# Kernel tuning notes

Hardware: AMD Instinct MI355X
Metric: run time of the kernel (lower is better)

## Reference

```python
import jax, jax.numpy as jnp
import numpy as np

T, B, C, HS, RD = 32, 32, 128, 512, 3  # timesteps, batch, state_channels, hidden_size, recurse_depth
HW = 7


def setup_inputs() -> dict:
    key = jax.random.key(0)
    ks = jax.random.split(key, 6)
    x = jax.random.normal(ks[0], (T * B, C, HW, HW), jnp.float32)
    hxs = jax.random.normal(ks[1], (B, 2 * C, HW, HW), jnp.float32)
    masks = jax.random.uniform(ks[2], (T * B,), jnp.float32)
    # ConvLSTMCell: conv over concat(x, h) [2C in] -> 4C gate channels, 3x3, bias
    Wconv = jax.random.normal(ks[3], (4 * C, 2 * C, 3, 3), jnp.float32) * 0.02
    bconv = jnp.zeros((4 * C,), jnp.float32)
    # flat_lin: Linear(C*7*7 -> hidden_size), torch layout [out, in]
    Wlin = jax.random.normal(ks[4], (HS, C * HW * HW), jnp.float32) * 0.02
    blin = jnp.zeros((HS,), jnp.float32)
    return {"x": x, "hxs": hxs, "masks": masks, "Wconv": Wconv, "bconv": bconv, "Wlin": Wlin, "blin": blin}


def reference(x, hxs, masks, Wconv, bconv, Wlin, blin):
    xs = x.reshape(T, B, C, HW, HW)
    ms = masks.reshape(T, B)
    h0, c0 = hxs[:, :C], hxs[:, C:]

    def conv_gates(inp):  # [B, 2C, 7, 7] -> [B, 4C, 7, 7]
        y = jax.lax.conv_general_dilated(
            inp, Wconv, window_strides=(1, 1), padding="SAME",
            dimension_numbers=("NCHW", "OIHW", "NCHW"))
        return y + bconv[None, :, None, None]

    def step(carry, inp):
        h, c = carry
        x_t, m_t = inp
        m = m_t[:, None, None, None]
        h = h * m
        c = c * m
        for _ in range(RD):  # recurse_depth inner unroll (sequential dependency)
            g = conv_gates(jnp.concatenate([x_t, h], axis=1))
            cc_i, cc_f, cc_o, cc_g = jnp.split(g, 4, axis=1)
            i = jax.nn.sigmoid(cc_i)
            f = jax.nn.sigmoid(cc_f)
            o = jax.nn.sigmoid(cc_o)
            gg = jnp.tanh(cc_g)
            c = f * c + i * gg
            h = o * jnp.tanh(c)
        out = jax.nn.relu(c.reshape(B, -1) @ Wlin.T + blin)  # flat_lin applied to c
        return (h, c), out

    (hT, cT), outs = jax.lax.scan(step, (h0, c0), (xs, ms))
    return outs.reshape(T * B, HS), jnp.concatenate([hT, cT], axis=1)
```

## Files before the change

### kernel.cpp

```cpp
#include <hip/hip_runtime.h>
#include <hip/hip_bf16.h>
#include <stdint.h>

#define T_  32
#define B_  32
#define C_  128
#define HS_ 512
#define HW_ 7
#define S_  49
#define CS_  (C_*S_)
#define ICS_ (2*C_*S_)
#define KH_  1152
#define KL_  6272
#define M_   1568
#define MR_  1600
#define N_   512

typedef __attribute__((ext_vector_type(8))) short short8;
typedef __attribute__((ext_vector_type(4))) float f32x4;
typedef __hip_bfloat16 bf16;

union bfbits { bf16 b; short s; };

__device__ __forceinline__ void gl16(const void* g, void* l) {
    __builtin_amdgcn_global_load_lds((const __attribute__((address_space(1))) void*)g,
                                     (__attribute__((address_space(3))) void*)l, 16, 0, 0);
}

__device__ __forceinline__ float sigm_f(float v) { return 1.0f / (1.0f + __expf(-v)); }
__device__ __forceinline__ float tanh_f(float v) { return 1.0f - 2.0f / (__expf(2.0f * v) + 1.0f); }

#define PIPE_BARRIER_COUNTED()  do {                                   \
    asm volatile("s_waitcnt vmcnt(8)" ::: "memory");                   \
    __builtin_amdgcn_sched_barrier(0);                                 \
    __builtin_amdgcn_s_barrier();                                      \
    __builtin_amdgcn_sched_barrier(0);                                 \
} while (0)
#define PIPE_BARRIER_DRAIN()  do {                                     \
    asm volatile("s_waitcnt vmcnt(0)" ::: "memory");                   \
    __builtin_amdgcn_sched_barrier(0);                                 \
    __builtin_amdgcn_s_barrier();                                      \
    __builtin_amdgcn_sched_barrier(0);                                 \
} while (0)

__global__ __launch_bounds__(256, 1) void k_fgemm(
    const bf16* __restrict__ xTt, const bf16* __restrict__ hT,
    bf16* __restrict__ hTN,
    const bf16* __restrict__ WxP, const bf16* __restrict__ WhP,
    const float* __restrict__ bconv,
    float* __restrict__ Gx, float* __restrict__ cbuf,
    const float* __restrict__ mask_c, const float* __restrict__ mask_a,
    bf16* __restrict__ chist_t, const bf16* __restrict__ zb, int mode0)
{
    __shared__ __align__(16) uint8_t smem[98304];
    bf16* sA = (bf16*)smem;
    bf16* sB = (bf16*)(smem + 49152);
    float (*gld)[68] = (float(*)[68])smem;

    const int tid = threadIdx.x, lane = tid & 63, w = tid >> 6;
    const int wr = w >> 1, wc = w & 1;
    const int m0 = blockIdx.x * 64, n0 = blockIdx.y * 64;

    const int kq = tid & 15, rr = tid >> 4;
    const int swz = ((kq ^ rr) << 3);
    int abS[4], ay[4], ax[4]; bool rok[4];
#pragma unroll
    for (int q = 0; q < 4; ++q) {
        int ra = m0 + q * 16 + rr;
        rok[q] = ra < M_;
        int b = ra / S_, s = ra - b * S_;
        abS[q] = b * S_;
        ay[q] = s / HW_; ax[q] = s - ay[q] * HW_;
    }

    const int NS = mode0 ? 18 : 9;

    f32x4 accX[2][2], accH[2][2];
    if (mode0) {
#pragma unroll
        for (int fn = 0; fn < 2; ++fn) {
            int np = n0 + wc * 32 + fn * 16 + (lane & 15);
            float bv = bconv[((np & 3) << 7) + (np >> 2)];
            f32x4 b4 = {bv, bv, bv, bv};
            accX[0][fn] = b4; accX[1][fn] = b4;
            f32x4 z4 = {0.f, 0.f, 0.f, 0.f};
            accH[0][fn] = z4; accH[1][fn] = z4;
        }
    } else {
#pragma unroll
        for (int fm = 0; fm < 2; ++fm) {
            int row = m0 + wr * 32 + fm * 16 + ((lane >> 4) << 2);
#pragma unroll
            for (int fn = 0; fn < 2; ++fn) {
                int col = n0 + wc * 32 + fn * 16 + (lane & 15);
#pragma unroll
                for (int j = 0; j < 4; ++j)
                    accH[fm][fn][j] = Gx[(size_t)(row + j) * N_ + col];
            }
        }
    }

    auto stage = [&](int st, int dbuf) {
        int xph = (mode0 && st < 9);
        int kid = xph ? st : (mode0 ? st - 9 : st);
        int ky = kid / 3, kx = kid - ky * 3;
        const bf16* Asrc = xph ? xTt : hT;
        const bf16* Wsrc = xph ? WxP : WhP;
        bf16* lA = sA + dbuf * 8192;
        bf16* lB = sB + dbuf * 8192;
#pragma unroll
        for (int q = 0; q < 4; ++q) {
            int y2 = ay[q] + ky - 1, x2 = ax[q] + kx - 1;
            const bf16* rb = (rok[q] && (unsigned)y2 < (unsigned)HW_ && (unsigned)x2 < (unsigned)HW_)
                ? Asrc + (((size_t)(abS[q] + y2 * HW_ + x2)) << 7) : zb;
            gl16(rb + swz, lA + q * 2048 + w * 512);
            gl16(Wsrc + (size_t)(n0 + q * 16 + rr) * KH_ + kid * 128 + swz, lB + q * 2048 + w * 512);
        }
    };

    auto compute = [&](int dbuf, f32x4 (&acc)[2][2]) {
        const bf16* lA = sA + dbuf * 8192;
        const bf16* lB = sB + dbuf * 8192;
        short8 af[2][4], bq[2][4];
#pragma unroll
        for (int kh = 0; kh < 4; ++kh) {
            int c = kh * 4 + (lane >> 4);
            int xr = (c ^ (lane & 15)) << 3;
#pragma unroll
            for (int fm = 0; fm < 2; ++fm) {
                int r = wr * 32 + fm * 16 + (lane & 15);
                af[fm][kh] = *(const short8*)(lA + r * 128 + xr);
            }
#pragma unroll
            for (int fn = 0; fn < 2; ++fn) {
                int r = wc * 32 + fn * 16 + (lane & 15);
                bq[fn][kh] = *(const short8*)(lB + r * 128 + xr);
            }
        }
#pragma unroll
        for (int kh = 0; kh < 4; ++kh)
#pragma unroll
            for (int fm = 0; fm < 2; ++fm)
#pragma unroll
                for (int fn = 0; fn < 2; ++fn)
                    acc[fm][fn] = __builtin_amdgcn_mfma_f32_16x16x32_bf16(
                        af[fm][kh], bq[fn][kh], acc[fm][fn], 0, 0, 0);
    };

    stage(0, 0);
    stage(1, 1);
    PIPE_BARRIER_COUNTED();

    int cur = 0;
#pragma unroll 1
    for (int st = 0; st < NS; ++st) {
        int pre = cur + 2; if (pre >= 3) pre -= 3;
        if (st + 2 < NS) stage(st + 2, pre);
        if (mode0 && st < 9) compute(cur, accX);
        else                 compute(cur, accH);
        if (st + 2 < NS) { PIPE_BARRIER_COUNTED(); }
        else             { PIPE_BARRIER_DRAIN(); }
        ++cur; if (cur == 3) cur = 0;
    }
    __syncthreads();

    if (mode0) {
#pragma unroll
        for (int fm = 0; fm < 2; ++fm) {
            int row = m0 + wr * 32 + fm * 16 + ((lane >> 4) << 2);
#pragma unroll
            for (int fn = 0; fn < 2; ++fn) {
                int col = n0 + wc * 32 + fn * 16 + (lane & 15);
#pragma unroll
                for (int j = 0; j < 4; ++j) {
                    Gx[(size_t)(row + j) * N_ + col] = accX[fm][fn][j];
                    accH[fm][fn][j] += accX[fm][fn][j];
                }
            }
        }
    }

#pragma unroll
    for (int fm = 0; fm < 2; ++fm)
#pragma unroll
        for (int fn = 0; fn < 2; ++fn) {
            int row = wr * 32 + fm * 16 + ((lane >> 4) << 2);
            int col = wc * 32 + fn * 16 + (lane & 15);
#pragma unroll
            for (int j = 0; j < 4; ++j) gld[row + j][col] = accH[fm][fn][j];
        }
    __syncthreads();

#pragma unroll
    for (int q2 = 0; q2 < 4; ++q2) {
        int e = tid + q2 * 256;
        int row = e >> 4, cc = e & 15;
        int m = m0 + row;
        if (m >= M_) continue;
        int b = m / S_, s = m - b * S_;
        int cg = (n0 >> 2) + cc;
        float g0 = gld[row][cc * 4 + 0], g1 = gld[row][cc * 4 + 1];
        float g2 = gld[row][cc * 4 + 2], g3 = gld[row][cc * 4 + 3];
        float ig = sigm_f(g0);
        float fg = sigm_f(g1);
        float og = sigm_f(g2);
        float gg = tanh_f(g3);
        size_t ci = (((size_t)b * S_ + s) << 7) + cg;
        float co = cbuf[ci];
        if (mask_c) co *= mask_c[b];
        float cn = fg * co + ig * gg;
        cbuf[ci] = cn;
        float hn = og * tanh_f(cn);
        float am = mask_a ? mask_a[b] : 1.f;
        hTN[ci] = __float2bfloat16(hn * am);
        if (chist_t) chist_t[(size_t)b * KL_ + s * C_ + cg] = __float2bfloat16(cn);
    }
}

__global__ __launch_bounds__(256, 1) void k_lingemm(
    const bf16* __restrict__ Ac, const bf16* __restrict__ Wl,
    const float* __restrict__ blin, float* __restrict__ out)
{
    __shared__ __align__(16) uint8_t smem[98304];
    bf16* sA = (bf16*)smem;
    bf16* sB = (bf16*)(smem + 49152);

    const int tid = threadIdx.x, lane = tid & 63, w = tid >> 6;
    const int wr = w >> 1, wc = w & 1;
    const int m0 = blockIdx.x * 64, n0 = blockIdx.y * 64;
    const int kq = tid & 15, rr = tid >> 4;
    const int swz = ((kq ^ rr) << 3);

    f32x4 acc[2][2];
#pragma unroll
    for (int fn = 0; fn < 2; ++fn) {
        int np = n0 + wc * 32 + fn * 16 + (lane & 15);
        float bv = blin[np];
        f32x4 b4 = {bv, bv, bv, bv};
        acc[0][fn] = b4; acc[1][fn] = b4;
    }

    auto stage = [&](int st, int dbuf) {
        bf16* lA = sA + dbuf * 8192;
        bf16* lB = sB + dbuf * 8192;
#pragma unroll
        for (int q = 0; q < 4; ++q) {
            gl16(Ac + (size_t)(m0 + q * 16 + rr) * KL_ + st * 128 + swz, lA + q * 2048 + w * 512);
            gl16(Wl + (size_t)(n0 + q * 16 + rr) * KL_ + st * 128 + swz, lB + q * 2048 + w * 512);
        }
    };
    auto compute = [&](int dbuf) {
        const bf16* lA = sA + dbuf * 8192;
        const bf16* lB = sB + dbuf * 8192;
        short8 af[2][4], bq[2][4];
#pragma unroll
        for (int kh = 0; kh < 4; ++kh) {
            int c = kh * 4 + (lane >> 4);
            int xr = (c ^ (lane & 15)) << 3;
#pragma unroll
            for (int fm = 0; fm < 2; ++fm) {
                int r = wr * 32 + fm * 16 + (lane & 15);
                af[fm][kh] = *(const short8*)(lA + r * 128 + xr);
            }
#pragma unroll
            for (int fn = 0; fn < 2; ++fn) {
                int r = wc * 32 + fn * 16 + (lane & 15);
                bq[fn][kh] = *(const short8*)(lB + r * 128 + xr);
            }
        }
#pragma unroll
        for (int kh = 0; kh < 4; ++kh)
#pragma unroll
            for (int fm = 0; fm < 2; ++fm)
#pragma unroll
                for (int fn = 0; fn < 2; ++fn)
                    acc[fm][fn] = __builtin_amdgcn_mfma_f32_16x16x32_bf16(
                        af[fm][kh], bq[fn][kh], acc[fm][fn], 0, 0, 0);
    };

    stage(0, 0);
    stage(1, 1);
    PIPE_BARRIER_COUNTED();

    int cur = 0;
#pragma unroll 1
    for (int st = 0; st < 49; ++st) {
        int pre = cur + 2; if (pre >= 3) pre -= 3;
        if (st + 2 < 49) stage(st + 2, pre);
        compute(cur);
        if (st + 2 < 49) { PIPE_BARRIER_COUNTED(); }
        else             { PIPE_BARRIER_DRAIN(); }
        ++cur; if (cur == 3) cur = 0;
    }

#pragma unroll
    for (int fm = 0; fm < 2; ++fm)
#pragma unroll
        for (int fn = 0; fn < 2; ++fn) {
            int col = n0 + wc * 32 + fn * 16 + (lane & 15);
            int rb  = m0 + wr * 32 + fm * 16 + ((lane >> 4) << 2);
#pragma unroll
            for (int j = 0; j < 4; ++j)
                out[(size_t)(rb + j) * N_ + col] = fmaxf(acc[fm][fn][j], 0.f);
        }
}

__global__ __launch_bounds__(256) void k_wsplit(const float* __restrict__ Wc,
                                               bf16* __restrict__ WxP, bf16* __restrict__ WhP) {
    int idx = blockIdx.x * 256 + threadIdx.x;
    if (idx >= 512 * 288) return;
    int np = idx / 288, kq = idx % 288;
    int oc = ((np & 3) << 7) + (np >> 2);
    int kk = kq * 8;
    int half = kk >= KH_;
    int krel = kk - half * KH_;
    short8 v;
#pragma unroll
    for (int j = 0; j < 8; ++j) {
        int kr = krel + j;
        int kid = kr >> 7, ic = (kr & 127) + half * 128;
        bfbits bb; bb.b = __float2bfloat16(Wc[((size_t)oc * 256 + ic) * 9 + kid]);
        v[j] = bb.s;
    }
    bf16* dst = half ? WhP : WxP;
    *reinterpret_cast<short8*>(dst + (size_t)np * KH_ + krel) = v;
}

__global__ __launch_bounds__(256) void k_wlin2(const float* __restrict__ Wl, bf16* __restrict__ Wp) {
    int idx = blockIdx.x * 256 + threadIdx.x;
    if (idx >= 512 * 784) return;
    int np = idx / 784, kq = idx % 784;
    short8 v;
#pragma unroll
    for (int j = 0; j < 8; ++j) {
        int kp = kq * 8 + j;
        int s = kp >> 7, c = kp & 127;
        bfbits bb; bb.b = __float2bfloat16(Wl[(size_t)np * KL_ + c * S_ + s]);
        v[j] = bb.s;
    }
    *reinterpret_cast<short8*>(Wp + (size_t)np * KL_ + kq * 8) = v;
}

__global__ __launch_bounds__(256) void k_xpose(const float* __restrict__ x, bf16* __restrict__ xT) {
    int idx = blockIdx.x * 256 + threadIdx.x;
    if (idx >= 1024 * 784) return;
    int r = idx / 784;
    int rem = idx % 784;
    int s = rem / 16, c8 = (rem & 15) * 8;
    const float* sp = x + (size_t)r * CS_ + c8 * S_ + s;
    short8 v;
#pragma unroll
    for (int j = 0; j < 8; ++j) { bfbits bb; bb.b = __float2bfloat16(sp[j * S_]); v[j] = bb.s; }
    *reinterpret_cast<short8*>(xT + (((size_t)r * S_ + s) << 7) + c8) = v;
}

__global__ __launch_bounds__(256) void k_hcprep(const float* __restrict__ hxs,
                                                const float* __restrict__ mask0,
                                                bf16* __restrict__ hT, float* __restrict__ cbuf) {
    int idx = blockIdx.x * 256 + threadIdx.x;
    if (idx >= 32 * 784) return;
    int b = idx / 784;
    int rem = idx % 784;
    int s = rem / 16, c8 = (rem & 15) * 8;
    float m = mask0[b];
    const float* hp = hxs + (size_t)b * ICS_ + c8 * S_ + s;
    const float* cp = hp + CS_;
    size_t o = (((size_t)b * S_ + s) << 7) + c8;
    short8 v;
#pragma unroll
    for (int j = 0; j < 8; ++j) {
        bfbits bb; bb.b = __float2bfloat16(hp[j * S_] * m); v[j] = bb.s;
        cbuf[o + j] = cp[j * S_];
    }
    *reinterpret_cast<short8*>(hT + o) = v;
}

__global__ __launch_bounds__(256) void k_zero16(uint4* __restrict__ p, int n) {
    int i = blockIdx.x * 256 + threadIdx.x;
    if (i < n) p[i] = make_uint4(0, 0, 0, 0);
}

__global__ __launch_bounds__(256) void k_final(const bf16* __restrict__ hT, const float* __restrict__ cbuf,
                                               float* __restrict__ out) {
    int i = blockIdx.x * 256 + threadIdx.x;
    if (i >= B_ * ICS_) return;
    int b = i / ICS_, r = i % ICS_;
    int ch = r / S_, s = r % S_;
    size_t o = (((size_t)b * S_ + s) << 7);
    out[i] = (ch < C_) ? __bfloat162float(hT[o + ch]) : cbuf[o + (ch - C_)];
}

extern "C" void kernel_launch(void* const* d_in, const int* in_sizes, int n_in,
                              void* d_out, int out_size, void* d_ws, size_t ws_size,
                              hipStream_t stream) {
    (void)in_sizes; (void)n_in; (void)out_size; (void)ws_size;
    const float* x     = (const float*)d_in[0];
    const float* hxs   = (const float*)d_in[1];
    const float* masks = (const float*)d_in[2];
    const float* Wconv = (const float*)d_in[3];
    const float* bconv = (const float*)d_in[4];
    const float* Wlin  = (const float*)d_in[5];
    const float* blin  = (const float*)d_in[6];
    float* out = (float*)d_out;

    uint8_t* p = (uint8_t*)d_ws;
    bf16* WxP   = (bf16*)p;   p += (size_t)512 * KH_ * 2;
    bf16* WhP   = (bf16*)p;   p += (size_t)512 * KH_ * 2;
    bf16* Wlp   = (bf16*)p;   p += (size_t)512 * KL_ * 2;
    bf16* xT    = (bf16*)p;   p += (size_t)1024 * S_ * C_ * 2;
    bf16* hA    = (bf16*)p;   p += (size_t)B_ * S_ * C_ * 2;
    bf16* hB    = (bf16*)p;   p += (size_t)B_ * S_ * C_ * 2;
    float* cbuf = (float*)p;  p += (size_t)B_ * S_ * C_ * 4;
    float* Gx   = (float*)p;  p += (size_t)MR_ * N_ * 4;
    bf16* chist = (bf16*)p;   p += (size_t)1024 * KL_ * 2;
    bf16* zb    = (bf16*)p;   p += 1024;
    bf16* hbufs[2] = {hA, hB};

    k_wsplit<<<576, 256, 0, stream>>>(Wconv, WxP, WhP);
    k_wlin2<<<1568, 256, 0, stream>>>(Wlin, Wlp);
    k_xpose<<<3136, 256, 0, stream>>>(x, xT);
    k_hcprep<<<98, 256, 0, stream>>>(hxs, masks, hA, cbuf);
    k_zero16<<<1, 256, 0, stream>>>((uint4*)zb, 64);

    int g = 0;
    for (int t = 0; t < T_; ++t) {
        const bf16* xTt = xT + (size_t)t * B_ * S_ * C_;
        for (int rd = 0; rd < 3; ++rd) {
            const float* mc = (rd == 0) ? masks + (size_t)t * B_ : nullptr;
            const float* ma = (rd == 2 && t < T_ - 1) ? masks + (size_t)(t + 1) * B_ : nullptr;
            bf16* ct = (rd == 2) ? chist + (size_t)t * B_ * KL_ : nullptr;
            k_fgemm<<<dim3(25, 8), 256, 0, stream>>>(
                (rd == 0) ? xTt : nullptr, hbufs[g & 1], hbufs[(g + 1) & 1],
                WxP, WhP, bconv, Gx, cbuf, mc, ma, ct, zb, (rd == 0) ? 1 : 0);
            ++g;
        }
    }

    k_lingemm<<<dim3(16, 8), 256, 0, stream>>>(chist, Wlp, blin, out);
    k_final<<<1568, 256, 0, stream>>>(hbufs[0], cbuf, out + (size_t)T_ * B_ * HS_);
}
```

Before: 1.464 ms.

## Replace per-step conv-LSTM launches with persistent kernel using grid barrier

Replaces the 96 separate fused conv-gate GEMM launches with one persistent kernel of 200 blocks. Each block keeps its slice of the recurrent weights resident in shared memory, holds its cell state and x-gate partial sums in registers, and synchronises with the other blocks through an atomic sense-reversing grid barrier. This removes per-launch overhead, the Gx round trips to global memory and re-staging of the weights on every step. In exchange the A operands now load directly from global memory without an LDS pipeline, and correctness relies on all 200 blocks being co-resident, since otherwise the spin barrier deadlocks.

```diff
diff --git a/kernel.cpp b/kernel.cpp
--- a/kernel.cpp
+++ b/kernel.cpp
@@ -13,8 +13,8 @@
 #define KH_  1152
 #define KL_  6272
 #define M_   1568
-#define MR_  1600
 #define N_   512
+#define NBLK_ 200
 
 typedef __attribute__((ext_vector_type(8))) short short8;
 typedef __attribute__((ext_vector_type(4))) float f32x4;
@@ -29,6 +29,231 @@
 
 __device__ __forceinline__ float sigm_f(float v) { return 1.0f / (1.0f + __expf(-v)); }
 __device__ __forceinline__ float tanh_f(float v) { return 1.0f - 2.0f / (__expf(2.0f * v) + 1.0f); }
+__device__ __forceinline__ float sel4(float r0, float r1, float r2, float r3, int idx) {
+    float a = (idx & 1) ? r1 : r0;
+    float b = (idx & 1) ? r3 : r2;
+    return (idx & 2) ? b : a;
+}
+
+__device__ __forceinline__ void grid_barrier(int* cnt, int* sense, int want) {
+    __threadfence();
+    __syncthreads();
+    if (threadIdx.x == 0) {
+        int v = __hip_atomic_fetch_add(cnt, 1, __ATOMIC_ACQ_REL, __HIP_MEMORY_SCOPE_AGENT);
+        if (v == NBLK_ - 1) {
+            __hip_atomic_store(cnt, 0, __ATOMIC_RELAXED, __HIP_MEMORY_SCOPE_AGENT);
+            __hip_atomic_store(sense, want, __ATOMIC_RELEASE, __HIP_MEMORY_SCOPE_AGENT);
+        } else {
+            while (__hip_atomic_load(sense, __ATOMIC_ACQUIRE, __HIP_MEMORY_SCOPE_AGENT) != want)
+                __builtin_amdgcn_s_sleep(16);
+        }
+    }
+    __syncthreads();
+}
+
+__global__ __launch_bounds__(256, 1) void k_persist(
+    const bf16* __restrict__ xT, bf16* __restrict__ h0, bf16* __restrict__ h1,
+    const bf16* __restrict__ WxP, const bf16* __restrict__ WhP,
+    const float* __restrict__ bconv, const float* __restrict__ cbuf,
+    const float* __restrict__ masks, bf16* __restrict__ chist,
+    float* __restrict__ outS, const bf16* __restrict__ zb, int* __restrict__ bar)
+{
+    __shared__ __align__(16) bf16 sWh[64 * KH_];
+
+    const int tid = threadIdx.x, lane = tid & 63, w = tid >> 6;
+    const int wr = w >> 1, wc = w & 1;
+    const int bid = blockIdx.x;
+    const int m0 = (bid >> 3) * 64, n0 = (bid & 7) * 64;
+
+#pragma unroll
+    for (int i = 0; i < 36; ++i) {
+        int ci = i * 256 + tid;
+        int col = ci / 144, s = ci - col * 144;
+        int sc = s ^ (col & 7);
+        gl16(WhP + (size_t)(n0 + col) * KH_ + sc * 8, sWh + (size_t)ci * 8);
+    }
+
+    int abase[2], ayy[2], axx[2]; bool aok[2];
+#pragma unroll
+    for (int fm = 0; fm < 2; ++fm) {
+        int ra = m0 + wr * 32 + fm * 16 + (lane & 15);
+        aok[fm] = ra < M_;
+        int b = ra / S_, s = ra - b * S_;
+        abase[fm] = b * S_;
+        ayy[fm] = s / HW_; axx[fm] = s - ayy[fm] * HW_;
+    }
+    const int aco = ((lane >> 4) << 3);
+
+    int ebc[2], esc[2], ebase[2]; bool eok[2];
+#pragma unroll
+    for (int fm = 0; fm < 2; ++fm) {
+        int er = m0 + wr * 32 + fm * 16 + ((lane >> 4) << 2) + (lane & 3);
+        eok[fm] = er < M_;
+        int b = er / S_, s = er - b * S_;
+        if (b > B_ - 1) b = B_ - 1;
+        ebc[fm] = b; esc[fm] = s; ebase[fm] = b * S_ + s;
+    }
+    int chn[2];
+#pragma unroll
+    for (int fn = 0; fn < 2; ++fn)
+        chn[fn] = (n0 >> 2) + wc * 8 + fn * 4 + ((lane & 15) >> 2);
+
+    float cst[2][2];
+#pragma unroll
+    for (int fm = 0; fm < 2; ++fm)
+#pragma unroll
+        for (int fn = 0; fn < 2; ++fn)
+            cst[fm][fn] = cbuf[((size_t)ebase[fm] << 7) + chn[fn]];
+
+    float bias[2];
+#pragma unroll
+    for (int fn = 0; fn < 2; ++fn) {
+        int np = n0 + wc * 32 + fn * 16 + (lane & 15);
+        bias[fn] = bconv[((np & 3) << 7) + (np >> 2)];
+    }
+
+    asm volatile("s_waitcnt vmcnt(0)" ::: "memory");
+    __syncthreads();
+
+    auto ldA = [&](const bf16* src, int kid, int fm, int kh) -> short8 {
+        int ky = kid / 3, kx = kid - 3 * (kid / 3);
+        int y2 = ayy[fm] + ky - 1, x2 = axx[fm] + kx - 1;
+        bool ok = aok[fm] && (unsigned)y2 < (unsigned)HW_ && (unsigned)x2 < (unsigned)HW_;
+        const bf16* p = ok ? src + (((size_t)(abase[fm] + y2 * HW_ + x2)) << 7) + kh * 32 + aco
+                           : zb;
+        return *(const short8*)p;
+    };
+    auto ldB = [&](int kid, int fn, int kh) -> short8 {
+        int col = wc * 32 + fn * 16 + (lane & 15);
+        int chunk = kid * 16 + kh * 4 + (lane >> 4);
+        int phys = chunk ^ (col & 7);
+        return *(const short8*)(sWh + col * KH_ + phys * 8);
+    };
+    auto ldBx = [&](int kid, int fn, int kh) -> short8 {
+        int col = n0 + wc * 32 + fn * 16 + (lane & 15);
+        return *(const short8*)(WxP + (size_t)col * KH_ + kid * 128 + kh * 32 + aco);
+    };
+
+    auto gemmH = [&](const bf16* hsrc, f32x4 (&acc)[2][2]) {
+#pragma unroll
+        for (int kid = 0; kid < 9; ++kid) {
+            short8 af[2][4], bq[2][4];
+#pragma unroll
+            for (int kh = 0; kh < 4; ++kh) {
+#pragma unroll
+                for (int fm = 0; fm < 2; ++fm) af[fm][kh] = ldA(hsrc, kid, fm, kh);
+#pragma unroll
+                for (int fn = 0; fn < 2; ++fn) bq[fn][kh] = ldB(kid, fn, kh);
+            }
+#pragma unroll
+            for (int kh = 0; kh < 4; ++kh)
+#pragma unroll
+                for (int fm = 0; fm < 2; ++fm)
+#pragma unroll
+                    for (int fn = 0; fn < 2; ++fn)
+                        acc[fm][fn] = __builtin_amdgcn_mfma_f32_16x16x32_bf16(
+                            af[fm][kh], bq[fn][kh], acc[fm][fn], 0, 0, 0);
+        }
+    };
+    auto gemmX = [&](const bf16* xsrc, f32x4 (&acc)[2][2]) {
+#pragma unroll
+        for (int kid = 0; kid < 9; ++kid) {
+            short8 af[2][4], bq[2][4];
+#pragma unroll
+            for (int kh = 0; kh < 4; ++kh) {
+#pragma unroll
+                for (int fm = 0; fm < 2; ++fm) af[fm][kh] = ldA(xsrc, kid, fm, kh);
+#pragma unroll
+                for (int fn = 0; fn < 2; ++fn) bq[fn][kh] = ldBx(kid, fn, kh);
+            }
+#pragma unroll
+            for (int kh = 0; kh < 4; ++kh)
+#pragma unroll
+                for (int fm = 0; fm < 2; ++fm)
+#pragma unroll
+                    for (int fn = 0; fn < 2; ++fn)
+                        acc[fm][fn] = __builtin_amdgcn_mfma_f32_16x16x32_bf16(
+                            af[fm][kh], bq[fn][kh], acc[fm][fn], 0, 0, 0);
+        }
+    };
+
+    const bf16* hcur = h0;
+    bf16* hnxt = h1;
+    f32x4 gx[2][2];
+    const int j = lane & 3;
+    int want = 1;
+
+#pragma unroll 1
+    for (int t = 0; t < T_; ++t) {
+        const bf16* xTt = xT + (size_t)t * (B_ * S_ * C_);
+#pragma unroll 1
+        for (int rd = 0; rd < 3; ++rd) {
+            f32x4 acc[2][2];
+            if (rd == 0) {
+#pragma unroll
+                for (int fm = 0; fm < 2; ++fm)
+#pragma unroll
+                    for (int fn = 0; fn < 2; ++fn) {
+                        f32x4 b4 = {bias[fn], bias[fn], bias[fn], bias[fn]};
+                        acc[fm][fn] = b4;
+                    }
+                gemmX(xTt, acc);
+#pragma unroll
+                for (int fm = 0; fm < 2; ++fm)
+#pragma unroll
+                    for (int fn = 0; fn < 2; ++fn) gx[fm][fn] = acc[fm][fn];
+                gemmH(hcur, acc);
+            } else {
+#pragma unroll
+                for (int fm = 0; fm < 2; ++fm)
+#pragma unroll
+                    for (int fn = 0; fn < 2; ++fn) acc[fm][fn] = gx[fm][fn];
+                gemmH(hcur, acc);
+            }
+
+            const bool last = (t == T_ - 1) && (rd == 2);
+#pragma unroll
+            for (int fm = 0; fm < 2; ++fm) {
+                float mc = 1.f, ma = 1.f;
+                if (rd == 0) mc = masks[t * B_ + ebc[fm]];
+                if (rd == 2 && t < T_ - 1) ma = masks[(t + 1) * B_ + ebc[fm]];
+#pragma unroll
+                for (int fn = 0; fn < 2; ++fn) {
+                    f32x4 a = acc[fm][fn];
+                    float s0 = sel4(a[0], a[1], a[2], a[3], j);
+                    float s1 = __shfl_xor(sel4(a[0], a[1], a[2], a[3], j ^ 1), 1);
+                    float s2 = __shfl_xor(sel4(a[0], a[1], a[2], a[3], j ^ 2), 2);
+                    float s3 = __shfl_xor(sel4(a[0], a[1], a[2], a[3], j ^ 3), 3);
+                    float gi = sel4(s0, s1, s2, s3, j);
+                    float gf = sel4(s0, s1, s2, s3, j ^ 1);
+                    float go = sel4(s0, s1, s2, s3, j ^ 2);
+                    float gg = sel4(s0, s1, s2, s3, j ^ 3);
+                    float ig = sigm_f(gi), fg = sigm_f(gf), og = sigm_f(go), gv = tanh_f(gg);
+                    float c = cst[fm][fn];
+                    if (rd == 0) c *= mc;
+                    float cn = fg * c + ig * gv;
+                    cst[fm][fn] = cn;
+                    float hn = og * tanh_f(cn);
+                    if (eok[fm]) {
+                        int ch = chn[fn];
+                        if (!last)
+                            hnxt[((size_t)ebase[fm] << 7) + ch] = __float2bfloat16(hn * ma);
+                        if (rd == 2)
+                            chist[((size_t)t * B_ + ebc[fm]) * KL_ + esc[fm] * C_ + ch] =
+                                __float2bfloat16(cn);
+                        if (last) {
+                            outS[(size_t)ebc[fm] * ICS_ + ch * S_ + esc[fm]] = hn;
+                            outS[(size_t)ebc[fm] * ICS_ + (C_ + ch) * S_ + esc[fm]] = cn;
+                        }
+                    }
+                }
+            }
+
+            if (!last) { grid_barrier(bar, bar + 1, want); want ^= 1; }
+            const bf16* tmp = hcur; hcur = hnxt; hnxt = (bf16*)tmp;
+        }
+    }
+}
 
 #define PIPE_BARRIER_COUNTED()  do {                                   \
     asm volatile("s_waitcnt vmcnt(8)" ::: "memory");                   \
@@ -43,180 +268,6 @@
     __builtin_amdgcn_sched_barrier(0);                                 \
 } while (0)
 
-__global__ __launch_bounds__(256, 1) void k_fgemm(
-    const bf16* __restrict__ xTt, const bf16* __restrict__ hT,
-    bf16* __restrict__ hTN,
-    const bf16* __restrict__ WxP, const bf16* __restrict__ WhP,
-    const float* __restrict__ bconv,
-    float* __restrict__ Gx, float* __restrict__ cbuf,
-    const float* __restrict__ mask_c, const float* __restrict__ mask_a,
-    bf16* __restrict__ chist_t, const bf16* __restrict__ zb, int mode0)
-{
-    __shared__ __align__(16) uint8_t smem[98304];
-    bf16* sA = (bf16*)smem;
-    bf16* sB = (bf16*)(smem + 49152);
-    float (*gld)[68] = (float(*)[68])smem;
-
-    const int tid = threadIdx.x, lane = tid & 63, w = tid >> 6;
-    const int wr = w >> 1, wc = w & 1;
-    const int m0 = blockIdx.x * 64, n0 = blockIdx.y * 64;
-
-    const int kq = tid & 15, rr = tid >> 4;
-    const int swz = ((kq ^ rr) << 3);
-    int abS[4], ay[4], ax[4]; bool rok[4];
-#pragma unroll
-    for (int q = 0; q < 4; ++q) {
-        int ra = m0 + q * 16 + rr;
-        rok[q] = ra < M_;
-        int b = ra / S_, s = ra - b * S_;
-        abS[q] = b * S_;
-        ay[q] = s / HW_; ax[q] = s - ay[q] * HW_;
-    }
-
-    const int NS = mode0 ? 18 : 9;
-
-    f32x4 accX[2][2], accH[2][2];
-    if (mode0) {
-#pragma unroll
-        for (int fn = 0; fn < 2; ++fn) {
-            int np = n0 + wc * 32 + fn * 16 + (lane & 15);
-            float bv = bconv[((np & 3) << 7) + (np >> 2)];
-            f32x4 b4 = {bv, bv, bv, bv};
-            accX[0][fn] = b4; accX[1][fn] = b4;
-            f32x4 z4 = {0.f, 0.f, 0.f, 0.f};
-            accH[0][fn] = z4; accH[1][fn] = z4;
-        }
-    } else {
-#pragma unroll
-        for (int fm = 0; fm < 2; ++fm) {
-            int row = m0 + wr * 32 + fm * 16 + ((lane >> 4) << 2);
-#pragma unroll
-            for (int fn = 0; fn < 2; ++fn) {
-                int col = n0 + wc * 32 + fn * 16 + (lane & 15);
-#pragma unroll
-                for (int j = 0; j < 4; ++j)
-                    accH[fm][fn][j] = Gx[(size_t)(row + j) * N_ + col];
-            }
-        }
-    }
-
-    auto stage = [&](int st, int dbuf) {
-        int xph = (mode0 && st < 9);
-        int kid = xph ? st : (mode0 ? st - 9 : st);
-        int ky = kid / 3, kx = kid - ky * 3;
-        const bf16* Asrc = xph ? xTt : hT;
-        const bf16* Wsrc = xph ? WxP : WhP;
-        bf16* lA = sA + dbuf * 8192;
-        bf16* lB = sB + dbuf * 8192;
-#pragma unroll
-        for (int q = 0; q < 4; ++q) {
-            int y2 = ay[q] + ky - 1, x2 = ax[q] + kx - 1;
-            const bf16* rb = (rok[q] && (unsigned)y2 < (unsigned)HW_ && (unsigned)x2 < (unsigned)HW_)
-                ? Asrc + (((size_t)(abS[q] + y2 * HW_ + x2)) << 7) : zb;
-            gl16(rb + swz, lA + q * 2048 + w * 512);
-            gl16(Wsrc + (size_t)(n0 + q * 16 + rr) * KH_ + kid * 128 + swz, lB + q * 2048 + w * 512);
-        }
-    };
-
-    auto compute = [&](int dbuf, f32x4 (&acc)[2][2]) {
-        const bf16* lA = sA + dbuf * 8192;
-        const bf16* lB = sB + dbuf * 8192;
-        short8 af[2][4], bq[2][4];
-#pragma unroll
-        for (int kh = 0; kh < 4; ++kh) {
-            int c = kh * 4 + (lane >> 4);
-            int xr = (c ^ (lane & 15)) << 3;
-#pragma unroll
-            for (int fm = 0; fm < 2; ++fm) {
-                int r = wr * 32 + fm * 16 + (lane & 15);
-                af[fm][kh] = *(const short8*)(lA + r * 128 + xr);
-            }
-#pragma unroll
-            for (int fn = 0; fn < 2; ++fn) {
-                int r = wc * 32 + fn * 16 + (lane & 15);
-                bq[fn][kh] = *(const short8*)(lB + r * 128 + xr);
-            }
-        }
-#pragma unroll
-        for (int kh = 0; kh < 4; ++kh)
-#pragma unroll
-            for (int fm = 0; fm < 2; ++fm)
-#pragma unroll
-                for (int fn = 0; fn < 2; ++fn)
-                    acc[fm][fn] = __builtin_amdgcn_mfma_f32_16x16x32_bf16(
-                        af[fm][kh], bq[fn][kh], acc[fm][fn], 0, 0, 0);
-    };
-
-    stage(0, 0);
-    stage(1, 1);
-    PIPE_BARRIER_COUNTED();
-
-    int cur = 0;
-#pragma unroll 1
-    for (int st = 0; st < NS; ++st) {
-        int pre = cur + 2; if (pre >= 3) pre -= 3;
-        if (st + 2 < NS) stage(st + 2, pre);
-        if (mode0 && st < 9) compute(cur, accX);
-        else                 compute(cur, accH);
-        if (st + 2 < NS) { PIPE_BARRIER_COUNTED(); }
-        else             { PIPE_BARRIER_DRAIN(); }
-        ++cur; if (cur == 3) cur = 0;
-    }
-    __syncthreads();
-
-    if (mode0) {
-#pragma unroll
-        for (int fm = 0; fm < 2; ++fm) {
-            int row = m0 + wr * 32 + fm * 16 + ((lane >> 4) << 2);
-#pragma unroll
-            for (int fn = 0; fn < 2; ++fn) {
-                int col = n0 + wc * 32 + fn * 16 + (lane & 15);
-#pragma unroll
-                for (int j = 0; j < 4; ++j) {
-                    Gx[(size_t)(row + j) * N_ + col] = accX[fm][fn][j];
-                    accH[fm][fn][j] += accX[fm][fn][j];
-                }
-            }
-        }
-    }
-
-#pragma unroll
-    for (int fm = 0; fm < 2; ++fm)
-#pragma unroll
-        for (int fn = 0; fn < 2; ++fn) {
-            int row = wr * 32 + fm * 16 + ((lane >> 4) << 2);
-            int col = wc * 32 + fn * 16 + (lane & 15);
-#pragma unroll
-            for (int j = 0; j < 4; ++j) gld[row + j][col] = accH[fm][fn][j];
-        }
-    __syncthreads();
-
-#pragma unroll
-    for (int q2 = 0; q2 < 4; ++q2) {
-        int e = tid + q2 * 256;
-        int row = e >> 4, cc = e & 15;
-        int m = m0 + row;
-        if (m >= M_) continue;
-        int b = m / S_, s = m - b * S_;
-        int cg = (n0 >> 2) + cc;
-        float g0 = gld[row][cc * 4 + 0], g1 = gld[row][cc * 4 + 1];
-        float g2 = gld[row][cc * 4 + 2], g3 = gld[row][cc * 4 + 3];
-        float ig = sigm_f(g0);
-        float fg = sigm_f(g1);
-        float og = sigm_f(g2);
-        float gg = tanh_f(g3);
-        size_t ci = (((size_t)b * S_ + s) << 7) + cg;
-        float co = cbuf[ci];
-        if (mask_c) co *= mask_c[b];
-        float cn = fg * co + ig * gg;
-        cbuf[ci] = cn;
-        float hn = og * tanh_f(cn);
-        float am = mask_a ? mask_a[b] : 1.f;
-        hTN[ci] = __float2bfloat16(hn * am);
-        if (chist_t) chist_t[(size_t)b * KL_ + s * C_ + cg] = __float2bfloat16(cn);
-    }
-}
-
 __global__ __launch_bounds__(256, 1) void k_lingemm(
     const bf16* __restrict__ Ac, const bf16* __restrict__ Wl,
     const float* __restrict__ blin, float* __restrict__ out)
@@ -300,8 +351,8 @@
             int col = n0 + wc * 32 + fn * 16 + (lane & 15);
             int rb  = m0 + wr * 32 + fm * 16 + ((lane >> 4) << 2);
 #pragma unroll
-            for (int j = 0; j < 4; ++j)
-                out[(size_t)(rb + j) * N_ + col] = fmaxf(acc[fm][fn][j], 0.f);
+            for (int jj = 0; jj < 4; ++jj)
+                out[(size_t)(rb + jj) * N_ + col] = fmaxf(acc[fm][fn][jj], 0.f);
         }
 }
 
@@ -316,11 +367,11 @@
     int krel = kk - half * KH_;
     short8 v;
 #pragma unroll
-    for (int j = 0; j < 8; ++j) {
-        int kr = krel + j;
+    for (int jj = 0; jj < 8; ++jj) {
+        int kr = krel + jj;
         int kid = kr >> 7, ic = (kr & 127) + half * 128;
         bfbits bb; bb.b = __float2bfloat16(Wc[((size_t)oc * 256 + ic) * 9 + kid]);
-        v[j] = bb.s;
+        v[jj] = bb.s;
     }
     bf16* dst = half ? WhP : WxP;
     *reinterpret_cast<short8*>(dst + (size_t)np * KH_ + krel) = v;
@@ -332,11 +383,11 @@
     int np = idx / 784, kq = idx % 784;
     short8 v;
 #pragma unroll
-    for (int j = 0; j < 8; ++j) {
-        int kp = kq * 8 + j;
+    for (int jj = 0; jj < 8; ++jj) {
+        int kp = kq * 8 + jj;
         int s = kp >> 7, c = kp & 127;
         bfbits bb; bb.b = __float2bfloat16(Wl[(size_t)np * KL_ + c * S_ + s]);
-        v[j] = bb.s;
+        v[jj] = bb.s;
     }
     *reinterpret_cast<short8*>(Wp + (size_t)np * KL_ + kq * 8) = v;
 }
@@ -350,7 +401,7 @@
     const float* sp = x + (size_t)r * CS_ + c8 * S_ + s;
     short8 v;
 #pragma unroll
-    for (int j = 0; j < 8; ++j) { bfbits bb; bb.b = __float2bfloat16(sp[j * S_]); v[j] = bb.s; }
+    for (int jj = 0; jj < 8; ++jj) { bfbits bb; bb.b = __float2bfloat16(sp[jj * S_]); v[jj] = bb.s; }
     *reinterpret_cast<short8*>(xT + (((size_t)r * S_ + s) << 7) + c8) = v;
 }
 
@@ -368,9 +419,9 @@
     size_t o = (((size_t)b * S_ + s) << 7) + c8;
     short8 v;
 #pragma unroll
-    for (int j = 0; j < 8; ++j) {
-        bfbits bb; bb.b = __float2bfloat16(hp[j * S_] * m); v[j] = bb.s;
-        cbuf[o + j] = cp[j * S_];
+    for (int jj = 0; jj < 8; ++jj) {
+        bfbits bb; bb.b = __float2bfloat16(hp[jj * S_] * m); v[jj] = bb.s;
+        cbuf[o + jj] = cp[jj * S_];
     }
     *reinterpret_cast<short8*>(hT + o) = v;
 }
@@ -378,16 +429,6 @@
 __global__ __launch_bounds__(256) void k_zero16(uint4* __restrict__ p, int n) {
     int i = blockIdx.x * 256 + threadIdx.x;
     if (i < n) p[i] = make_uint4(0, 0, 0, 0);
-}
-
-__global__ __launch_bounds__(256) void k_final(const bf16* __restrict__ hT, const float* __restrict__ cbuf,
-                                               float* __restrict__ out) {
-    int i = blockIdx.x * 256 + threadIdx.x;
-    if (i >= B_ * ICS_) return;
-    int b = i / ICS_, r = i % ICS_;
-    int ch = r / S_, s = r % S_;
-    size_t o = (((size_t)b * S_ + s) << 7);
-    out[i] = (ch < C_) ? __bfloat162float(hT[o + ch]) : cbuf[o + (ch - C_)];
 }
 
 extern "C" void kernel_launch(void* const* d_in, const int* in_sizes, int n_in,
@@ -411,31 +452,19 @@
     bf16* hA    = (bf16*)p;   p += (size_t)B_ * S_ * C_ * 2;
     bf16* hB    = (bf16*)p;   p += (size_t)B_ * S_ * C_ * 2;
     float* cbuf = (float*)p;  p += (size_t)B_ * S_ * C_ * 4;
-    float* Gx   = (float*)p;  p += (size_t)MR_ * N_ * 4;
     bf16* chist = (bf16*)p;   p += (size_t)1024 * KL_ * 2;
     bf16* zb    = (bf16*)p;   p += 1024;
-    bf16* hbufs[2] = {hA, hB};
+    int*  bar   = (int*)p;    p += 1024;
 
     k_wsplit<<<576, 256, 0, stream>>>(Wconv, WxP, WhP);
     k_wlin2<<<1568, 256, 0, stream>>>(Wlin, Wlp);
     k_xpose<<<3136, 256, 0, stream>>>(x, xT);
     k_hcprep<<<98, 256, 0, stream>>>(hxs, masks, hA, cbuf);
-    k_zero16<<<1, 256, 0, stream>>>((uint4*)zb, 64);
-
-    int g = 0;
-    for (int t = 0; t < T_; ++t) {
-        const bf16* xTt = xT + (size_t)t * B_ * S_ * C_;
-        for (int rd = 0; rd < 3; ++rd) {
-            const float* mc = (rd == 0) ? masks + (size_t)t * B_ : nullptr;
-            const float* ma = (rd == 2 && t < T_ - 1) ? masks + (size_t)(t + 1) * B_ : nullptr;
-            bf16* ct = (rd == 2) ? chist + (size_t)t * B_ * KL_ : nullptr;
-            k_fgemm<<<dim3(25, 8), 256, 0, stream>>>(
-                (rd == 0) ? xTt : nullptr, hbufs[g & 1], hbufs[(g + 1) & 1],
-                WxP, WhP, bconv, Gx, cbuf, mc, ma, ct, zb, (rd == 0) ? 1 : 0);
-            ++g;
-        }
-    }
+    k_zero16<<<1, 256, 0, stream>>>((uint4*)zb, 128);
+
+    k_persist<<<dim3(NBLK_), dim3(256), 0, stream>>>(
+        xT, hA, hB, WxP, WhP, bconv, cbuf, masks, chist,
+        out + (size_t)T_ * B_ * HS_, zb, bar);
 
     k_lingemm<<<dim3(16, 8), 256, 0, stream>>>(chist, Wlp, blin, out);
-    k_final<<<1568, 256, 0, stream>>>(hbufs[0], cbuf, out + (size_t)T_ * B_ * HS_);
-}
+}
```

Result: slower. 4.905 ms (+235.1%).

## Stage whole batch-row halo in LDS and read weights directly from global

Applied to the files above, without the earlier changes.

Each block now loads all input rows for its batches (up to 147 spatial rows plus a zero row) into LDS once, instead of doing a per-tap im2col gather through a triple-buffered pipeline. The 3x3 taps then index LDS directly. Weights are read straight from global/L2 into registers rather than staged through LDS. The gate epilogue uses lane shuffles in place of an LDS round trip, and the separate zero-buffer kernel is removed. The risks are exposed global weight-load latency with no software pipelining, and a larger LDS footprint that may change occupancy.

```diff
diff --git a/kernel.cpp b/kernel.cpp
--- a/kernel.cpp
+++ b/kernel.cpp
@@ -15,6 +15,7 @@
 #define M_   1568
 #define MR_  1600
 #define N_   512
+#define ZROW_ 147
 
 typedef __attribute__((ext_vector_type(8))) short short8;
 typedef __attribute__((ext_vector_type(4))) float f32x4;
@@ -29,6 +30,178 @@
 
 __device__ __forceinline__ float sigm_f(float v) { return 1.0f / (1.0f + __expf(-v)); }
 __device__ __forceinline__ float tanh_f(float v) { return 1.0f - 2.0f / (__expf(2.0f * v) + 1.0f); }
+__device__ __forceinline__ float sel4(float r0, float r1, float r2, float r3, int idx) {
+    float a = (idx & 1) ? r1 : r0;
+    float b = (idx & 1) ? r3 : r2;
+    return (idx & 2) ? b : a;
+}
+
+__global__ __launch_bounds__(256) void k_fgemm(
+    const bf16* __restrict__ xTt, const bf16* __restrict__ hT,
+    bf16* __restrict__ hTN,
+    const bf16* __restrict__ WxP, const bf16* __restrict__ WhP,
+    const float* __restrict__ bconv,
+    float* __restrict__ Gx, float* __restrict__ cbuf,
+    const float* __restrict__ mask_c, const float* __restrict__ mask_a,
+    bf16* __restrict__ chist_t, int mode0)
+{
+    __shared__ __align__(16) bf16 sH[148 * 128];
+    __shared__ __align__(16) bf16 sX[148 * 128];
+
+    const int tid = threadIdx.x, lane = tid & 63, w = tid >> 6;
+    const int wr = w >> 1, wc = w & 1;
+    const int m0 = blockIdx.x * 64, n0 = blockIdx.y * 64;
+    const int bA = m0 / S_;
+
+#pragma unroll
+    for (int i = 0; i < 10; ++i) {
+        int ci = i * 256 + tid;
+        if (ci < 2352) {
+            int rl = ci >> 4, q = ci & 15;
+            int grow = bA * S_ + rl; if (grow > M_ - 1) grow = M_ - 1;
+            gl16(hT + ((size_t)grow << 7) + ((q ^ (rl & 15)) << 3), sH + (size_t)ci * 8);
+        }
+    }
+    if (mode0) {
+#pragma unroll
+        for (int i = 0; i < 10; ++i) {
+            int ci = i * 256 + tid;
+            if (ci < 2352) {
+                int rl = ci >> 4, q = ci & 15;
+                int grow = bA * S_ + rl; if (grow > M_ - 1) grow = M_ - 1;
+                gl16(xTt + ((size_t)grow << 7) + ((q ^ (rl & 15)) << 3), sX + (size_t)ci * 8);
+            }
+        }
+    }
+    if (tid < 16) *(short8*)(sH + ZROW_ * 128 + tid * 8) = short8{0,0,0,0,0,0,0,0};
+    else if (tid < 32) *(short8*)(sX + ZROW_ * 128 + (tid - 16) * 8) = short8{0,0,0,0,0,0,0,0};
+    asm volatile("s_waitcnt vmcnt(0)" ::: "memory");
+    __syncthreads();
+
+    int rbl[2], ayy[2], axx[2]; bool aok[2];
+#pragma unroll
+    for (int fm = 0; fm < 2; ++fm) {
+        int ra = m0 + wr * 32 + fm * 16 + (lane & 15);
+        aok[fm] = ra < M_;
+        int rc = aok[fm] ? ra : 0;
+        int b = rc / S_, s = rc - b * S_;
+        rbl[fm] = (b - bA) * S_;
+        ayy[fm] = s / HW_; axx[fm] = s - ayy[fm] * HW_;
+    }
+
+    auto ldA = [&](const bf16* buf, int kid, int fm, int kh) -> short8 {
+        int ky = kid / 3, kx = kid - 3 * (kid / 3);
+        int y2 = ayy[fm] + ky - 1, x2 = axx[fm] + kx - 1;
+        bool ok = aok[fm] && (unsigned)y2 < (unsigned)HW_ && (unsigned)x2 < (unsigned)HW_;
+        int rl = ok ? rbl[fm] + y2 * HW_ + x2 : ZROW_;
+        int chunk = kh * 4 + (lane >> 4);
+        return *(const short8*)(buf + rl * 128 + ((chunk ^ (rl & 15)) << 3));
+    };
+    auto ldW = [&](const bf16* W, int kid, int fn, int kh) -> short8 {
+        int col = n0 + wc * 32 + fn * 16 + (lane & 15);
+        return *(const short8*)(W + (size_t)col * KH_ + kid * 128 + kh * 32 + ((lane >> 4) << 3));
+    };
+
+    auto gemm = [&](const bf16* Abuf, const bf16* W, f32x4 (&acc)[2][2]) {
+#pragma unroll
+        for (int kid = 0; kid < 9; ++kid) {
+            short8 af[2][4], bq[2][4];
+#pragma unroll
+            for (int kh = 0; kh < 4; ++kh) {
+#pragma unroll
+                for (int fm = 0; fm < 2; ++fm) af[fm][kh] = ldA(Abuf, kid, fm, kh);
+#pragma unroll
+                for (int fn = 0; fn < 2; ++fn) bq[fn][kh] = ldW(W, kid, fn, kh);
+            }
+#pragma unroll
+            for (int kh = 0; kh < 4; ++kh)
+#pragma unroll
+                for (int fm = 0; fm < 2; ++fm)
+#pragma unroll
+                    for (int fn = 0; fn < 2; ++fn)
+                        acc[fm][fn] = __builtin_amdgcn_mfma_f32_16x16x32_bf16(
+                            af[fm][kh], bq[fn][kh], acc[fm][fn], 0, 0, 0);
+        }
+    };
+
+    f32x4 accH[2][2];
+    if (mode0) {
+        f32x4 accX[2][2];
+#pragma unroll
+        for (int fn = 0; fn < 2; ++fn) {
+            int np = n0 + wc * 32 + fn * 16 + (lane & 15);
+            float bv = bconv[((np & 3) << 7) + (np >> 2)];
+            f32x4 b4 = {bv, bv, bv, bv};
+            accX[0][fn] = b4; accX[1][fn] = b4;
+            f32x4 z4 = {0.f, 0.f, 0.f, 0.f};
+            accH[0][fn] = z4; accH[1][fn] = z4;
+        }
+        gemm(sX, WxP, accX);
+        gemm(sH, WhP, accH);
+#pragma unroll
+        for (int fm = 0; fm < 2; ++fm) {
+            int row = m0 + wr * 32 + fm * 16 + ((lane >> 4) << 2);
+#pragma unroll
+            for (int fn = 0; fn < 2; ++fn) {
+                int col = n0 + wc * 32 + fn * 16 + (lane & 15);
+#pragma unroll
+                for (int j = 0; j < 4; ++j) {
+                    Gx[(size_t)(row + j) * N_ + col] = accX[fm][fn][j];
+                    accH[fm][fn][j] += accX[fm][fn][j];
+                }
+            }
+        }
+    } else {
+#pragma unroll
+        for (int fm = 0; fm < 2; ++fm) {
+            int row = m0 + wr * 32 + fm * 16 + ((lane >> 4) << 2);
+#pragma unroll
+            for (int fn = 0; fn < 2; ++fn) {
+                int col = n0 + wc * 32 + fn * 16 + (lane & 15);
+#pragma unroll
+                for (int j = 0; j < 4; ++j)
+                    accH[fm][fn][j] = Gx[(size_t)(row + j) * N_ + col];
+            }
+        }
+        gemm(sH, WhP, accH);
+    }
+
+    const int j = lane & 3;
+#pragma unroll
+    for (int fm = 0; fm < 2; ++fm) {
+        int er = m0 + wr * 32 + fm * 16 + ((lane >> 4) << 2) + (lane & 3);
+        bool eok = er < M_;
+        int rc = eok ? er : 0;
+        int eb = rc / S_, es = rc - eb * S_;
+        float mc = mask_c ? mask_c[eb] : 1.f;
+        float ma = mask_a ? mask_a[eb] : 1.f;
+#pragma unroll
+        for (int fn = 0; fn < 2; ++fn) {
+            int chn = (n0 >> 2) + wc * 8 + fn * 4 + ((lane & 15) >> 2);
+            f32x4 a = accH[fm][fn];
+            float s0 = sel4(a[0], a[1], a[2], a[3], j);
+            float s1 = __shfl_xor(sel4(a[0], a[1], a[2], a[3], j ^ 1), 1);
+            float s2 = __shfl_xor(sel4(a[0], a[1], a[2], a[3], j ^ 2), 2);
+            float s3 = __shfl_xor(sel4(a[0], a[1], a[2], a[3], j ^ 3), 3);
+            float gi = sel4(s0, s1, s2, s3, j);
+            float gf = sel4(s0, s1, s2, s3, j ^ 1);
+            float go = sel4(s0, s1, s2, s3, j ^ 2);
+            float gg = sel4(s0, s1, s2, s3, j ^ 3);
+            float ig = sigm_f(gi), fg = sigm_f(gf), og = sigm_f(go), gv = tanh_f(gg);
+            if (eok) {
+                size_t ci = (((size_t)(eb * S_ + es)) << 7) + chn;
+                float c = cbuf[ci];
+                if (mask_c) c *= mc;
+                float cn = fg * c + ig * gv;
+                cbuf[ci] = cn;
+                float hn = og * tanh_f(cn);
+                hTN[ci] = __float2bfloat16(hn * ma);
+                if (chist_t)
+                    chist_t[(size_t)eb * KL_ + es * C_ + chn] = __float2bfloat16(cn);
+            }
+        }
+    }
+}
 
 #define PIPE_BARRIER_COUNTED()  do {                                   \
     asm volatile("s_waitcnt vmcnt(8)" ::: "memory");                   \
@@ -43,180 +216,6 @@
     __builtin_amdgcn_sched_barrier(0);                                 \
 } while (0)
 
-__global__ __launch_bounds__(256, 1) void k_fgemm(
-    const bf16* __restrict__ xTt, const bf16* __restrict__ hT,
-    bf16* __restrict__ hTN,
-    const bf16* __restrict__ WxP, const bf16* __restrict__ WhP,
-    const float* __restrict__ bconv,
-    float* __restrict__ Gx, float* __restrict__ cbuf,
-    const float* __restrict__ mask_c, const float* __restrict__ mask_a,
-    bf16* __restrict__ chist_t, const bf16* __restrict__ zb, int mode0)
-{
-    __shared__ __align__(16) uint8_t smem[98304];
-    bf16* sA = (bf16*)smem;
-    bf16* sB = (bf16*)(smem + 49152);
-    float (*gld)[68] = (float(*)[68])smem;
-
-    const int tid = threadIdx.x, lane = tid & 63, w = tid >> 6;
-    const int wr = w >> 1, wc = w & 1;
-    const int m0 = blockIdx.x * 64, n0 = blockIdx.y * 64;
-
-    const int kq = tid & 15, rr = tid >> 4;
-    const int swz = ((kq ^ rr) << 3);
-    int abS[4], ay[4], ax[4]; bool rok[4];
-#pragma unroll
-    for (int q = 0; q < 4; ++q) {
-        int ra = m0 + q * 16 + rr;
-        rok[q] = ra < M_;
-        int b = ra / S_, s = ra - b * S_;
-        abS[q] = b * S_;
-        ay[q] = s / HW_; ax[q] = s - ay[q] * HW_;
-    }
-
-    const int NS = mode0 ? 18 : 9;
-
-    f32x4 accX[2][2], accH[2][2];
-    if (mode0) {
-#pragma unroll
-        for (int fn = 0; fn < 2; ++fn) {
-            int np = n0 + wc * 32 + fn * 16 + (lane & 15);
-            float bv = bconv[((np & 3) << 7) + (np >> 2)];
-            f32x4 b4 = {bv, bv, bv, bv};
-            accX[0][fn] = b4; accX[1][fn] = b4;
-            f32x4 z4 = {0.f, 0.f, 0.f, 0.f};
-            accH[0][fn] = z4; accH[1][fn] = z4;
-        }
-    } else {
-#pragma unroll
-        for (int fm = 0; fm < 2; ++fm) {
-            int row = m0 + wr * 32 + fm * 16 + ((lane >> 4) << 2);
-#pragma unroll
-            for (int fn = 0; fn < 2; ++fn) {
-                int col = n0 + wc * 32 + fn * 16 + (lane & 15);
-#pragma unroll
-                for (int j = 0; j < 4; ++j)
-                    accH[fm][fn][j] = Gx[(size_t)(row + j) * N_ + col];
-            }
-        }
-    }
-
-    auto stage = [&](int st, int dbuf) {
-        int xph = (mode0 && st < 9);
-        int kid = xph ? st : (mode0 ? st - 9 : st);
-        int ky = kid / 3, kx = kid - ky * 3;
-        const bf16* Asrc = xph ? xTt : hT;
-        const bf16* Wsrc = xph ? WxP : WhP;
-        bf16* lA = sA + dbuf * 8192;
-        bf16* lB = sB + dbuf * 8192;
-#pragma unroll
-        for (int q = 0; q < 4; ++q) {
-            int y2 = ay[q] + ky - 1, x2 = ax[q] + kx - 1;
-            const bf16* rb = (rok[q] && (unsigned)y2 < (unsigned)HW_ && (unsigned)x2 < (unsigned)HW_)
-                ? Asrc + (((size_t)(abS[q] + y2 * HW_ + x2)) << 7) : zb;
-            gl16(rb + swz, lA + q * 2048 + w * 512);
-            gl16(Wsrc + (size_t)(n0 + q * 16 + rr) * KH_ + kid * 128 + swz, lB + q * 2048 + w * 512);
-        }
-    };
-
-    auto compute = [&](int dbuf, f32x4 (&acc)[2][2]) {
-        const bf16* lA = sA + dbuf * 8192;
-        const bf16* lB = sB + dbuf * 8192;
-        short8 af[2][4], bq[2][4];
-#pragma unroll
-        for (int kh = 0; kh < 4; ++kh) {
-            int c = kh * 4 + (lane >> 4);
-            int xr = (c ^ (lane & 15)) << 3;
-#pragma unroll
-            for (int fm = 0; fm < 2; ++fm) {
-                int r = wr * 32 + fm * 16 + (lane & 15);
-                af[fm][kh] = *(const short8*)(lA + r * 128 + xr);
-            }
-#pragma unroll
-            for (int fn = 0; fn < 2; ++fn) {
-                int r = wc * 32 + fn * 16 + (lane & 15);
-                bq[fn][kh] = *(const short8*)(lB + r * 128 + xr);
-            }
-        }
-#pragma unroll
-        for (int kh = 0; kh < 4; ++kh)
-#pragma unroll
-            for (int fm = 0; fm < 2; ++fm)
-#pragma unroll
-                for (int fn = 0; fn < 2; ++fn)
-                    acc[fm][fn] = __builtin_amdgcn_mfma_f32_16x16x32_bf16(
-                        af[fm][kh], bq[fn][kh], acc[fm][fn], 0, 0, 0);
-    };
-
-    stage(0, 0);
-    stage(1, 1);
-    PIPE_BARRIER_COUNTED();
-
-    int cur = 0;
-#pragma unroll 1
-    for (int st = 0; st < NS; ++st) {
-        int pre = cur + 2; if (pre >= 3) pre -= 3;
-        if (st + 2 < NS) stage(st + 2, pre);
-        if (mode0 && st < 9) compute(cur, accX);
-        else                 compute(cur, accH);
-        if (st + 2 < NS) { PIPE_BARRIER_COUNTED(); }
-        else             { PIPE_BARRIER_DRAIN(); }
-        ++cur; if (cur == 3) cur = 0;
-    }
-    __syncthreads();
-
-    if (mode0) {
-#pragma unroll
-        for (int fm = 0; fm < 2; ++fm) {
-            int row = m0 + wr * 32 + fm * 16 + ((lane >> 4) << 2);
-#pragma unroll
-            for (int fn = 0; fn < 2; ++fn) {
-                int col = n0 + wc * 32 + fn * 16 + (lane & 15);
-#pragma unroll
-                for (int j = 0; j < 4; ++j) {
-                    Gx[(size_t)(row + j) * N_ + col] = accX[fm][fn][j];
-                    accH[fm][fn][j] += accX[fm][fn][j];
-                }
-            }
-        }
-    }
-
-#pragma unroll
-    for (int fm = 0; fm < 2; ++fm)
-#pragma unroll
-        for (int fn = 0; fn < 2; ++fn) {
-            int row = wr * 32 + fm * 16 + ((lane >> 4) << 2);
-            int col = wc * 32 + fn * 16 + (lane & 15);
-#pragma unroll
-            for (int j = 0; j < 4; ++j) gld[row + j][col] = accH[fm][fn][j];
-        }
-    __syncthreads();
-
-#pragma unroll
-    for (int q2 = 0; q2 < 4; ++q2) {
-        int e = tid + q2 * 256;
-        int row = e >> 4, cc = e & 15;
-        int m = m0 + row;
-        if (m >= M_) continue;
-        int b = m / S_, s = m - b * S_;
-        int cg = (n0 >> 2) + cc;
-        float g0 = gld[row][cc * 4 + 0], g1 = gld[row][cc * 4 + 1];
-        float g2 = gld[row][cc * 4 + 2], g3 = gld[row][cc * 4 + 3];
-        float ig = sigm_f(g0);
-        float fg = sigm_f(g1);
-        float og = sigm_f(g2);
-        float gg = tanh_f(g3);
-        size_t ci = (((size_t)b * S_ + s) << 7) + cg;
-        float co = cbuf[ci];
-        if (mask_c) co *= mask_c[b];
-        float cn = fg * co + ig * gg;
-        cbuf[ci] = cn;
-        float hn = og * tanh_f(cn);
-        float am = mask_a ? mask_a[b] : 1.f;
-        hTN[ci] = __float2bfloat16(hn * am);
-        if (chist_t) chist_t[(size_t)b * KL_ + s * C_ + cg] = __float2bfloat16(cn);
-    }
-}
-
 __global__ __launch_bounds__(256, 1) void k_lingemm(
     const bf16* __restrict__ Ac, const bf16* __restrict__ Wl,
     const float* __restrict__ blin, float* __restrict__ out)
@@ -300,8 +299,8 @@
             int col = n0 + wc * 32 + fn * 16 + (lane & 15);
             int rb  = m0 + wr * 32 + fm * 16 + ((lane >> 4) << 2);
 #pragma unroll
-            for (int j = 0; j < 4; ++j)
-                out[(size_t)(rb + j) * N_ + col] = fmaxf(acc[fm][fn][j], 0.f);
+            for (int jj = 0; jj < 4; ++jj)
+                out[(size_t)(rb + jj) * N_ + col] = fmaxf(acc[fm][fn][jj], 0.f);
         }
 }
 
@@ -316,11 +315,11 @@
     int krel = kk - half * KH_;
     short8 v;
 #pragma unroll
-    for (int j = 0; j < 8; ++j) {
-        int kr = krel + j;
+    for (int jj = 0; jj < 8; ++jj) {
+        int kr = krel + jj;
         int kid = kr >> 7, ic = (kr & 127) + half * 128;
         bfbits bb; bb.b = __float2bfloat16(Wc[((size_t)oc * 256 + ic) * 9 + kid]);
-        v[j] = bb.s;
+        v[jj] = bb.s;
     }
     bf16* dst = half ? WhP : WxP;
     *reinterpret_cast<short8*>(dst + (size_t)np * KH_ + krel) = v;
@@ -332,11 +331,11 @@
     int np = idx / 784, kq = idx % 784;
     short8 v;
 #pragma unroll
-    for (int j = 0; j < 8; ++j) {
-        int kp = kq * 8 + j;
+    for (int jj = 0; jj < 8; ++jj) {
+        int kp = kq * 8 + jj;
         int s = kp >> 7, c = kp & 127;
         bfbits bb; bb.b = __float2bfloat16(Wl[(size_t)np * KL_ + c * S_ + s]);
-        v[j] = bb.s;
+        v[jj] = bb.s;
     }
     *reinterpret_cast<short8*>(Wp + (size_t)np * KL_ + kq * 8) = v;
 }
@@ -350,7 +349,7 @@
     const float* sp = x + (size_t)r * CS_ + c8 * S_ + s;
     short8 v;
 #pragma unroll
-    for (int j = 0; j < 8; ++j) { bfbits bb; bb.b = __float2bfloat16(sp[j * S_]); v[j] = bb.s; }
+    for (int jj = 0; jj < 8; ++jj) { bfbits bb; bb.b = __float2bfloat16(sp[jj * S_]); v[jj] = bb.s; }
     *reinterpret_cast<short8*>(xT + (((size_t)r * S_ + s) << 7) + c8) = v;
 }
 
@@ -368,16 +367,11 @@
     size_t o = (((size_t)b * S_ + s) << 7) + c8;
     short8 v;
 #pragma unroll
-    for (int j = 0; j < 8; ++j) {
-        bfbits bb; bb.b = __float2bfloat16(hp[j * S_] * m); v[j] = bb.s;
-        cbuf[o + j] = cp[j * S_];
+    for (int jj = 0; jj < 8; ++jj) {
+        bfbits bb; bb.b = __float2bfloat16(hp[jj * S_] * m); v[jj] = bb.s;
+        cbuf[o + jj] = cp[jj * S_];
     }
     *reinterpret_cast<short8*>(hT + o) = v;
-}
-
-__global__ __launch_bounds__(256) void k_zero16(uint4* __restrict__ p, int n) {
-    int i = blockIdx.x * 256 + threadIdx.x;
-    if (i < n) p[i] = make_uint4(0, 0, 0, 0);
 }
 
 __global__ __launch_bounds__(256) void k_final(const bf16* __restrict__ hT, const float* __restrict__ cbuf,
@@ -413,14 +407,12 @@
     float* cbuf = (float*)p;  p += (size_t)B_ * S_ * C_ * 4;
     float* Gx   = (float*)p;  p += (size_t)MR_ * N_ * 4;
     bf16* chist = (bf16*)p;   p += (size_t)1024 * KL_ * 2;
-    bf16* zb    = (bf16*)p;   p += 1024;
     bf16* hbufs[2] = {hA, hB};
 
     k_wsplit<<<576, 256, 0, stream>>>(Wconv, WxP, WhP);
     k_wlin2<<<1568, 256, 0, stream>>>(Wlin, Wlp);
     k_xpose<<<3136, 256, 0, stream>>>(x, xT);
     k_hcprep<<<98, 256, 0, stream>>>(hxs, masks, hA, cbuf);
-    k_zero16<<<1, 256, 0, stream>>>((uint4*)zb, 64);
 
     int g = 0;
     for (int t = 0; t < T_; ++t) {
@@ -431,7 +423,7 @@
             bf16* ct = (rd == 2) ? chist + (size_t)t * B_ * KL_ : nullptr;
             k_fgemm<<<dim3(25, 8), 256, 0, stream>>>(
                 (rd == 0) ? xTt : nullptr, hbufs[g & 1], hbufs[(g + 1) & 1],
-                WxP, WhP, bconv, Gx, cbuf, mc, ma, ct, zb, (rd == 0) ? 1 : 0);
+                WxP, WhP, bconv, Gx, cbuf, mc, ma, ct, (rd == 0) ? 1 : 0);
             ++g;
         }
     }
```

After: 1.596 ms. 9.0% more time.
